# Performance work log

Measured on AMD Instinct MI355X. Metric: run time of the kernel, lower is better.

The kernel has to match this reference:

```python
import jax, jax.numpy as jnp
import numpy as np

B, T, E = 2, 2048, 2048
H, NOPE, ROPE, VD, KVR, DR = 16, 64, 32, 64, 256, 2
QKD = NOPE + ROPE  # 96
LOWR = KVR // 4    # hypernet low_rank=4 -> 64


def _rope_angles(position, dim):
    # freqs_cis angles: pos * 10000^(-2i/dim), matching torch rotary with theta=10000
    inv = jnp.exp(jnp.arange(0, dim, 2, dtype=jnp.float32) * (-jnp.log(jnp.float32(10000.0)) / dim))
    return position.astype(jnp.float32)[..., None] * inv  # (1, T, dim//2)


def _apply_rotary(x, ang):
    # x: (B,T,H,D); pairs are consecutive elements (view_as_complex semantics)
    x2 = x.reshape(x.shape[:-1] + (-1, 2))
    c = jnp.cos(ang)[:, :, None, :]
    s = jnp.sin(ang)[:, :, None, :]
    xr, xi = x2[..., 0], x2[..., 1]
    return jnp.stack([xr * c - xi * s, xr * s + xi * c], axis=-1).reshape(x.shape)


def _layernorm(x, g, b, eps=1e-5):
    m = jnp.mean(x, axis=-1, keepdims=True)
    v = jnp.var(x, axis=-1, keepdims=True)
    return (x - m) * jax.lax.rsqrt(v + eps) * g + b


def _sinusoid_pe(t, d):
    pos = jnp.arange(t, dtype=jnp.float32)[:, None]
    div = jnp.exp(jnp.arange(0, d, 2, dtype=jnp.float32) * (-jnp.log(jnp.float32(10000.0)) / d))
    pe = jnp.zeros((t, d), dtype=jnp.float32)
    pe = pe.at[:, 0::2].set(jnp.sin(pos * div)).at[:, 1::2].set(jnp.cos(pos * div))
    return pe


def setup_inputs() -> dict:
    key = jax.random.key(0)
    ks = jax.random.split(key, 16)
    sd = 0.02
    return {
        "query": jax.random.normal(ks[0], (B, T, E), jnp.float32),
        "key": jax.random.normal(ks[1], (B, T, E), jnp.float32),
        "value": jax.random.normal(ks[2], (B, T, E), jnp.float32),
        "position": jnp.arange(T, dtype=jnp.int32)[None, :],
        # weights stored transposed for right-multiply (x @ W)
        "wq": jax.random.normal(ks[3], (E, H * QKD), jnp.float32) * sd,
        "wkv_a": jax.random.normal(ks[4], (E, KVR + ROPE), jnp.float32) * sd,
        "kv_gamma": jnp.ones((KVR,), jnp.float32),
        "kv_beta": jnp.zeros((KVR,), jnp.float32),
        # torch layout (H*(NOPE+VD), KVR) kept for faithful view(H,-1,KVR) absorb
        "wkv_b": jax.random.normal(ks[5], (H * (NOPE + VD), KVR), jnp.float32) * sd,
        "wo": jax.random.normal(ks[6], (H * VD, E), jnp.float32) * sd,
        "fc_c_w": jax.random.normal(ks[7], (KVR, LOWR), jnp.float32) * sd,
        "fc_c_b": jnp.zeros((LOWR,), jnp.float32),
        "fc_p_w": jax.random.normal(ks[8], (KVR, LOWR), jnp.float32) * sd,
        "fc_p_b": jnp.zeros((LOWR,), jnp.float32),
    }


def reference(query, key, value, position, wq, wkv_a, kv_gamma, kv_beta, wkv_b, wo,
              fc_c_w, fc_c_b, fc_p_w, fc_p_b):
    bsz, seqlen, _ = query.shape
    # queries: low-rank-free path (q_lora_rank=0)
    q = (query @ wq).reshape(bsz, seqlen, H, QKD)
    q_nope, q_pe = q[..., :NOPE], q[..., NOPE:]
    ang = _rope_angles(position, ROPE)  # (1, T, ROPE//2)
    q_pe = _apply_rotary(q_pe, ang[:, -seqlen:])
    # key/value latent projection
    kv_all = key @ wkv_a  # (B, T, KVR+ROPE)
    kv, k_pe = kv_all[..., :KVR], kv_all[..., KVR:]
    k_pe = _apply_rotary(k_pe[:, :, None, :], ang)[:, :, 0, :]  # (B, T, ROPE)
    kv_norm = _layernorm(kv, kv_gamma, kv_beta)  # (B, T, KVR)
    # hypernetwork temporal downsampling weights (train path, T_input=kv_norm)
    t = -(-seqlen // DR)
    C = jnp.repeat(_sinusoid_pe(t, KVR), DR, axis=0)[:seqlen]  # (T, KVR)
    C2 = C @ fc_c_w + fc_c_b           # (T, LOWR)
    P2 = kv_norm @ fc_p_w + fc_p_b     # (B, T, LOWR)
    W = jax.nn.sigmoid(jnp.einsum('tc,bsc->bts', C2, P2))  # (B, T, T)
    idx = jnp.arange(seqlen)
    chunk = idx // DR
    # chunk mask: cumulative within-chunk causal accumulation
    zero_mask = ((chunk[:, None] == chunk[None, :]) & (idx[None, :] <= idx[:, None])).astype(query.dtype)
    kv_t = jnp.einsum('bts,bsc->btc', W * zero_mask, kv_norm)  # (B, T, KVR)
    # stride-aware causal mask: attend completed chunk-end slots + own in-progress slot
    allowed = (idx[None, :] == idx[:, None]) | ((idx[None, :] < idx[:, None]) & (((idx[None, :] + 1) % DR) == 0))
    attn_mask = jnp.where(allowed, jnp.float32(0.0), jnp.float32(-1e30))
    # absorbed MLA attention
    wb = wkv_b.reshape(H, NOPE + VD, KVR)
    q_abs = jnp.einsum('bshd,hdc->bshc', q_nope, wb[:, :NOPE])  # (B, S, H, KVR)
    scores = (jnp.einsum('bshc,btc->bsht', q_abs, kv_t)
              + jnp.einsum('bshr,btr->bsht', q_pe, k_pe)) * (QKD ** -0.5)
    scores = scores + attn_mask[None, :, None, :]
    attn = jax.nn.softmax(scores, axis=-1)
    x = jnp.einsum('bsht,btc->bshc', attn, kv_t)
    x = jnp.einsum('bshc,hdc->bshd', x, wb[:, NOPE:])  # (B, S, H, VD)
    return x.reshape(bsz, seqlen, H * VD) @ wo
```

## Files before the change

kernel.cpp:

```cpp
#include <hip/hip_runtime.h>
#include <stddef.h>

typedef unsigned short u16;
typedef unsigned short u16x8 __attribute__((ext_vector_type(8)));
typedef short s16x8 __attribute__((ext_vector_type(8)));
typedef float f32x4 __attribute__((ext_vector_type(4)));

#define B_ 2
#define T_ 2048
#define E_ 2048
#define H_ 16

__device__ inline float us2f(u16 u){
  unsigned int i = ((unsigned int)u) << 16;
  return __builtin_bit_cast(float, i);
}
__device__ inline u16 f2us(float f){
  unsigned int x = __builtin_bit_cast(unsigned int, f);
  unsigned int r = (x + 0x7fffu + ((x >> 16) & 1u)) >> 16;
  return (u16)r;
}
__device__ inline f32x4 mfma32(s16x8 a, s16x8 b, f32x4 c){
  return __builtin_amdgcn_mfma_f32_16x16x32_bf16(a, b, c, 0, 0, 0);
}
__device__ inline s16x8 ld8(const u16* p){
  return __builtin_bit_cast(s16x8, *(const u16x8*)p);
}
__device__ inline void gload_lds16(const u16* g, u16* l){
  __builtin_amdgcn_global_load_lds(
      (const __attribute__((address_space(1))) unsigned int*)(g),
      (__attribute__((address_space(3))) unsigned int*)(l), 16, 0, 0);
}

__global__ __launch_bounds__(256) void prep_weights(
    const float* __restrict__ wq, const float* __restrict__ wkva,
    const float* __restrict__ wo, const float* __restrict__ wkvb,
    u16* __restrict__ wqT, u16* __restrict__ wkvaT, u16* __restrict__ woT,
    u16* __restrict__ wkvbB)
{
  __shared__ float tile[32][33];
  const int bid = blockIdx.x;
  const int tid = threadIdx.x;
  if (bid < 5696) {
    const float* in; u16* out; int R, C, bx, by;
    if (bid < 3072)      { in = wq;   out = wqT;   R = 2048; C = 1536; bx = bid % 48;          by = bid / 48; }
    else if (bid < 3648) { in = wkva; out = wkvaT; R = 2048; C = 288;  bx = (bid-3072) % 9;    by = (bid-3072) / 9; }
    else                 { in = wo;   out = woT;   R = 1024; C = 2048; bx = (bid-3648) % 64;   by = (bid-3648) / 64; }
    int tx = tid & 31, ty = tid >> 5;
    int c0 = bx * 32, r0 = by * 32;
    for (int i = ty; i < 32; i += 8){
      int r = r0 + i, c = c0 + tx;
      tile[i][tx] = (r < R && c < C) ? in[(size_t)r * C + c] : 0.f;
    }
    __syncthreads();
    for (int i = ty; i < 32; i += 8){
      int c = c0 + i, r = r0 + tx;
      if (c < C && r < R) out[(size_t)c * R + r] = f2us(tile[tx][i]);
    }
  } else {
    int i = (bid - 5696) * 1024 + tid * 4;
    f32x4 v = *(const f32x4*)(wkvb + i);
    wkvbB[i]   = f2us(v[0]); wkvbB[i+1] = f2us(v[1]);
    wkvbB[i+2] = f2us(v[2]); wkvbB[i+3] = f2us(v[3]);
  }
}

__global__ __launch_bounds__(256) void cvt2_f32_bf16(const float* __restrict__ a,
    const float* __restrict__ b, u16* __restrict__ oa, u16* __restrict__ ob, int n_each)
{
  int idx = (blockIdx.x * 256 + threadIdx.x) * 4;
  const float* in; u16* out; int i;
  if (idx < n_each){ in = a; out = oa; i = idx; }
  else             { in = b; out = ob; i = idx - n_each; }
  if (i + 3 < n_each){
    f32x4 v = *(const f32x4*)(in + i);
    out[i]   = f2us(v[0]); out[i+1] = f2us(v[1]);
    out[i+2] = f2us(v[2]); out[i+3] = f2us(v[3]);
  }
}

template<int A_F32, int OUT_F32>
__global__ __launch_bounds__(256) void gemm_bt(const void* __restrict__ Ap,
    const u16* __restrict__ Bt, void* __restrict__ Cp, int M, int N, int K)
{
  __shared__ __align__(16) u16 As[64][40];
  __shared__ __align__(16) u16 Bs[64][40];
  const int tid  = threadIdx.x;
  const int lane = tid & 63;
  const int wid  = tid >> 6;
  const int quad = lane >> 4;
  const int col  = lane & 15;
  const int bm = blockIdx.y * 64;
  const int bn = blockIdx.x * 64;
  const int lr = tid >> 2;
  const int lc = (tid & 3) * 8;
  const int waveM = wid >> 1, waveN = wid & 1;

  f32x4 acc[2][2];
  for (int i = 0; i < 2; ++i)
    for (int j = 0; j < 2; ++j)
      acc[i][j] = (f32x4){0.f, 0.f, 0.f, 0.f};

  const u16x8 zero8 = {0,0,0,0,0,0,0,0};
  const bool bok = (bn + lr) < N;
  const u16*   arow16 = (const u16*)Ap   + (size_t)(bm + lr) * K + lc;
  const float* arow32 = (const float*)Ap + (size_t)(bm + lr) * K + lc;
  const u16* brow = Bt + (size_t)(bn + lr) * K + lc;

  for (int kk = 0; kk < K; kk += 32) {
    u16x8 av;
    if (A_F32) {
      f32x4 a0 = *(const f32x4*)(arow32 + kk);
      f32x4 a1 = *(const f32x4*)(arow32 + kk + 4);
      av[0]=f2us(a0[0]); av[1]=f2us(a0[1]); av[2]=f2us(a0[2]); av[3]=f2us(a0[3]);
      av[4]=f2us(a1[0]); av[5]=f2us(a1[1]); av[6]=f2us(a1[2]); av[7]=f2us(a1[3]);
    } else {
      av = *(const u16x8*)(arow16 + kk);
    }
    u16x8 bv = bok ? *(const u16x8*)(brow + kk) : zero8;
    __syncthreads();
    *(u16x8*)&As[lr][lc] = av;
    *(u16x8*)&Bs[lr][lc] = bv;
    __syncthreads();
    s16x8 af0 = ld8(&As[waveM*32 + col][quad*8]);
    s16x8 af1 = ld8(&As[waveM*32 + 16 + col][quad*8]);
    s16x8 bf0 = ld8(&Bs[waveN*32 + col][quad*8]);
    s16x8 bf1 = ld8(&Bs[waveN*32 + 16 + col][quad*8]);
    acc[0][0] = mfma32(af0, bf0, acc[0][0]);
    acc[0][1] = mfma32(af0, bf1, acc[0][1]);
    acc[1][0] = mfma32(af1, bf0, acc[1][0]);
    acc[1][1] = mfma32(af1, bf1, acc[1][1]);
  }
  for (int am = 0; am < 2; ++am)
    for (int bnn = 0; bnn < 2; ++bnn)
      for (int i = 0; i < 4; ++i) {
        int r = bm + waveM*32 + am*16 + quad*4 + i;
        int c = bn + waveN*32 + bnn*16 + col;
        if (c < N){
          if (OUT_F32) ((float*)Cp)[(size_t)r * N + c] = acc[am][bnn][i];
          else         ((u16*)Cp)[(size_t)r * N + c]   = f2us(acc[am][bnn][i]);
        }
      }
}

template<int OUT_F32>
__global__ __launch_bounds__(256) void gemm128(const u16* __restrict__ A,
    const u16* __restrict__ Bt, void* __restrict__ Cp, int M, int N, int K)
{
  __shared__ __align__(16) u16 As[128 * 32];
  __shared__ __align__(16) u16 Bs[128 * 32];
  const int tid  = threadIdx.x;
  const int lane = tid & 63;
  const int wid  = tid >> 6;
  const int quad = lane >> 4;
  const int col  = lane & 15;
  const int bm = blockIdx.y * 128;
  const int bn = blockIdx.x * 128;
  const int waveM = wid >> 1, waveN = wid & 1;

  const int srow = wid * 16 + (lane >> 2);
  const int scol = (lane & 3) * 8;
  const u16* ga = A  + (size_t)(bm + srow) * K + scol;
  const u16* gb = Bt + (size_t)(bn + srow) * K + scol;
  const size_t rowskip = (size_t)64 * K;
  u16* lAs0 = &As[wid * 512];
  u16* lAs1 = &As[wid * 512 + 2048];
  u16* lBs0 = &Bs[wid * 512];
  u16* lBs1 = &Bs[wid * 512 + 2048];

  f32x4 acc[4][4] = {};

  for (int kk = 0; kk < K; kk += 32) {
    __syncthreads();
    gload_lds16(ga + kk,           lAs0);
    gload_lds16(ga + rowskip + kk, lAs1);
    gload_lds16(gb + kk,           lBs0);
    gload_lds16(gb + rowskip + kk, lBs1);
    __syncthreads();
    s16x8 af[4], bf[4];
#pragma unroll
    for (int i = 0; i < 4; ++i) af[i] = ld8(&As[(waveM*64 + i*16 + col) * 32 + quad*8]);
#pragma unroll
    for (int i = 0; i < 4; ++i) bf[i] = ld8(&Bs[(waveN*64 + i*16 + col) * 32 + quad*8]);
#pragma unroll
    for (int i = 0; i < 4; ++i)
#pragma unroll
      for (int j = 0; j < 4; ++j)
        acc[i][j] = mfma32(af[i], bf[j], acc[i][j]);
  }
#pragma unroll
  for (int i = 0; i < 4; ++i)
#pragma unroll
    for (int j = 0; j < 4; ++j)
#pragma unroll
      for (int r = 0; r < 4; ++r) {
        int row = bm + waveM*64 + i*16 + quad*4 + r;
        int c   = bn + waveN*64 + j*16 + col;
        if (OUT_F32) ((float*)Cp)[(size_t)row * N + c] = acc[i][j][r];
        else         ((u16*)Cp)[(size_t)row * N + c]   = f2us(acc[i][j][r]);
      }
}

__global__ __launch_bounds__(256) void gemm128_sk(const u16* __restrict__ A,
    const u16* __restrict__ Bt, u16* __restrict__ Cp0, u16* __restrict__ Cp1,
    int M, int N, int K, int Klen)
{
  __shared__ __align__(16) u16 As[128 * 32];
  __shared__ __align__(16) u16 Bs[128 * 32];
  const int tid  = threadIdx.x;
  const int lane = tid & 63;
  const int wid  = tid >> 6;
  const int quad = lane >> 4;
  const int col  = lane & 15;
  const int bm = blockIdx.y * 128;
  const int bn = blockIdx.x * 128;
  const int kh = blockIdx.z;
  const int waveM = wid >> 1, waveN = wid & 1;

  const int srow = wid * 16 + (lane >> 2);
  const int scol = (lane & 3) * 8;
  const u16* ga = A  + (size_t)(bm + srow) * K + kh * Klen + scol;
  const u16* gb = Bt + (size_t)(bn + srow) * K + kh * Klen + scol;
  const size_t rowskip = (size_t)64 * K;
  u16* lAs0 = &As[wid * 512];
  u16* lAs1 = &As[wid * 512 + 2048];
  u16* lBs0 = &Bs[wid * 512];
  u16* lBs1 = &Bs[wid * 512 + 2048];
  u16* Cp = kh ? Cp1 : Cp0;

  f32x4 acc[4][4] = {};

  for (int kk = 0; kk < Klen; kk += 32) {
    __syncthreads();
    gload_lds16(ga + kk,           lAs0);
    gload_lds16(ga + rowskip + kk, lAs1);
    gload_lds16(gb + kk,           lBs0);
    gload_lds16(gb + rowskip + kk, lBs1);
    __syncthreads();
    s16x8 af[4], bf[4];
#pragma unroll
    for (int i = 0; i < 4; ++i) af[i] = ld8(&As[(waveM*64 + i*16 + col) * 32 + quad*8]);
#pragma unroll
    for (int i = 0; i < 4; ++i) bf[i] = ld8(&Bs[(waveN*64 + i*16 + col) * 32 + quad*8]);
#pragma unroll
    for (int i = 0; i < 4; ++i)
#pragma unroll
      for (int j = 0; j < 4; ++j)
        acc[i][j] = mfma32(af[i], bf[j], acc[i][j]);
  }
#pragma unroll
  for (int i = 0; i < 4; ++i)
#pragma unroll
    for (int j = 0; j < 4; ++j)
#pragma unroll
      for (int r = 0; r < 4; ++r) {
        int row = bm + waveM*64 + i*16 + quad*4 + r;
        int c   = bn + waveN*64 + j*16 + col;
        Cp[(size_t)row * N + c] = f2us(acc[i][j][r]);
      }
}

__global__ __launch_bounds__(256) void qsplit(const u16* __restrict__ qp0,
    const u16* __restrict__ qp1, const int* __restrict__ pos, u16* __restrict__ qh)
{
  int idx = blockIdx.x * 256 + threadIdx.x;
  if (idx >= B_*T_*H_*12) return;
  int c    = idx % 12;
  int rest = idx / 12;
  int h    = rest & 15;
  int row  = rest >> 4;
  int t    = row & (T_ - 1);
  int b    = row >> 11;
  size_t off = (size_t)row * 1536 + h * 96 + c * 8;
  u16x8 v0 = *(const u16x8*)(qp0 + off);
  u16x8 v1 = *(const u16x8*)(qp1 + off);
  u16x8 v;
  if (c < 8) {
#pragma unroll
    for (int k = 0; k < 8; ++k) v[k] = f2us(us2f(v0[k]) + us2f(v1[k]));
  } else {
    int i0 = (c - 8) * 4;
    float pp = (float)pos[t];
#pragma unroll
    for (int k = 0; k < 4; ++k){
      int i = i0 + k;
      float ang = pp * __expf((float)(2*i) * -0.28782313657f);
      float cs = __cosf(ang), sn = __sinf(ang);
      float xr = us2f(v0[2*k])   + us2f(v1[2*k]);
      float xi = us2f(v0[2*k+1]) + us2f(v1[2*k+1]);
      v[2*k]   = f2us(xr * cs - xi * sn);
      v[2*k+1] = f2us(xr * sn + xi * cs);
    }
  }
  u16* dst = qh + ((size_t)(b * 16 + h) * T_ + t) * 96;
  *(u16x8*)(dst + c * 8) = v;
}

__global__ __launch_bounds__(256) void ln_p2_rope(
    const u16* __restrict__ kvall, const float* __restrict__ gamma,
    const float* __restrict__ beta, const float* __restrict__ fcpw,
    const float* __restrict__ fcpb, const int* __restrict__ pos,
    u16* __restrict__ kvn, float* __restrict__ P2, u16* __restrict__ kpe)
{
  const int row = blockIdx.x;
  if (row >= B_ * T_) return;
  const int tid = threadIdx.x;
  const int lane = tid & 63, wid = tid >> 6;
  __shared__ float kvs[256];
  __shared__ float part[256];
  __shared__ float redS[4], redS2[4];
  const u16* src = kvall + (size_t)row * 288;
  float v = us2f(src[tid]);
  float s1 = v, s2 = v * v;
  for (int off = 1; off < 64; off <<= 1){
    s1 += __shfl_xor(s1, off);
    s2 += __shfl_xor(s2, off);
  }
  if (lane == 0){ redS[wid] = s1; redS2[wid] = s2; }
  __syncthreads();
  float S  = redS[0] + redS[1] + redS[2] + redS[3];
  float Q  = redS2[0] + redS2[1] + redS2[2] + redS2[3];
  float mean = S * (1.f / 256.f);
  float var  = Q * (1.f / 256.f) - mean * mean;
  float rstd = rsqrtf(var + 1e-5f);
  float xn = (v - mean) * rstd * gamma[tid] + beta[tid];
  kvs[tid] = xn;
  kvn[(size_t)row * 256 + tid] = f2us(xn);
  __syncthreads();
  {
    int oc = tid & 63, pp = tid >> 6;
    float acc = 0.f;
#pragma unroll 8
    for (int c = pp * 64; c < pp * 64 + 64; ++c)
      acc += kvs[c] * fcpw[c * 64 + oc];
    part[tid] = acc;
  }
  __syncthreads();
  if (tid < 64) {
    P2[(size_t)row * 64 + tid] = fcpb[tid] + part[tid] + part[64 + tid]
                               + part[128 + tid] + part[192 + tid];
  } else if (tid < 80) {
    int i = tid - 64;
    int t = row & (T_ - 1);
    float ang = (float)pos[t] * __expf((float)(2*i) * -0.28782313657f);
    float c = __cosf(ang), s = __sinf(ang);
    float xr = us2f(src[256 + 2*i]);
    float xi = us2f(src[257 + 2*i]);
    kpe[(size_t)row * 32 + 2*i]     = f2us(xr * c - xi * s);
    kpe[(size_t)row * 32 + 2*i + 1] = f2us(xr * s + xi * c);
  }
}

__global__ __launch_bounds__(256) void c2_kernel(const float* __restrict__ fccw,
    const float* __restrict__ fccb, float* __restrict__ C2)
{
  const int t = blockIdx.x, tid = threadIdx.x;
  __shared__ float pe[256];
  __shared__ float part[256];
  float p = (float)(t >> 1);
  if (tid < 128){
    float div = __expf((float)(2*tid) * -0.03597789207f);
    float a = p * div;
    pe[2*tid]   = __sinf(a);
    pe[2*tid+1] = __cosf(a);
  }
  __syncthreads();
  {
    int oc = tid & 63, pp = tid >> 6;
    float acc = 0.f;
#pragma unroll 8
    for (int c = pp * 64; c < pp * 64 + 64; ++c)
      acc += pe[c] * fccw[c * 64 + oc];
    part[tid] = acc;
  }
  __syncthreads();
  if (tid < 64)
    C2[t * 64 + tid] = fccb[tid] + part[tid] + part[64 + tid]
                     + part[128 + tid] + part[192 + tid];
}

__global__ __launch_bounds__(64) void kvt_kernel(const float* __restrict__ C2,
    const float* __restrict__ P2, const u16* __restrict__ kvn, u16* __restrict__ kvt)
{
  const int row = blockIdx.x;
  if (row >= B_ * T_) return;
  const int lane = threadIdx.x;
  const int t = row & (T_ - 1);
  float c2v = C2[t * 64 + lane];
  float da = c2v * P2[(size_t)row * 64 + lane];
  for (int off = 1; off < 64; off <<= 1) da += __shfl_xor(da, off);
  float wtt = 1.f / (1.f + __expf(-da));
  const bool odd = (t & 1);
  float wts = 0.f;
  if (odd){
    float db = c2v * P2[(size_t)(row - 1) * 64 + lane];
    for (int off = 1; off < 64; off <<= 1) db += __shfl_xor(db, off);
    wts = 1.f / (1.f + __expf(-db));
  }
  for (int c = lane; c < 256; c += 64){
    float val = wtt * us2f(kvn[(size_t)row * 256 + c]);
    if (odd) val += wts * us2f(kvn[(size_t)(row - 1) * 256 + c]);
    kvt[(size_t)row * 256 + c] = f2us(val);
  }
}

__global__ __launch_bounds__(256) void vtkc_kernel(const u16* __restrict__ kvb,
    const u16* __restrict__ kpe, u16* __restrict__ Vt, u16* __restrict__ Kc)
{
  __shared__ __align__(16) u16 tile[64][72];
  const int tid = threadIdx.x;
  if (blockIdx.x < 512) {
    const int bid = blockIdx.x;
    const int jt = bid & 15;
    const int h  = (bid >> 4) & 15;
    const int b  = bid >> 8;
    const int jl = tid >> 2;
    const int dseg = (tid & 3) * 16;
    const int j0 = jt * 64;
    {
      int s_ = 2 * (j0 + jl) + 1;
      const u16* src = kvb + ((size_t)(b * T_ + s_)) * 2048 + h * 128 + 64 + dseg;
      *(u16x8*)&tile[jl][dseg]     = *(const u16x8*)(src);
      *(u16x8*)&tile[jl][dseg + 8] = *(const u16x8*)(src + 8);
    }
    __syncthreads();
    const int dl = tid >> 2;
    const int jseg = (tid & 3) * 16;
    u16* dst = Vt + ((size_t)(b * 16 + h) * 64 + dl) * 1024 + j0 + jseg;
    u16x8 o;
    for (int r = 0; r < 8; ++r) o[r] = tile[jseg + r][dl];
    *(u16x8*)dst = o;
    for (int r = 0; r < 8; ++r) o[r] = tile[jseg + 8 + r][dl];
    *(u16x8*)(dst + 8) = o;
  } else {
    int idx = (blockIdx.x - 512) * 256 + tid;
    int c  = idx % 12;
    int j  = (idx / 12) & 1023;
    int bh = idx / (12 * 1024);
    if (bh >= B_ * H_) return;
    int b = bh >> 4, h = bh & 15;
    int t = 2 * j + 1;
    u16x8 v;
    if (c < 8) v = *(const u16x8*)(kvb + ((size_t)(b * T_ + t)) * 2048 + h * 128 + c * 8);
    else       v = *(const u16x8*)(kpe + ((size_t)(b * T_ + t)) * 32 + (c - 8) * 8);
    *(u16x8*)(Kc + ((size_t)bh * 1024 + j) * 96 + c * 8) = v;
  }
}

__global__ __launch_bounds__(256) void attn_kernel(
    const u16* __restrict__ qh, const u16* __restrict__ kvb,
    const u16* __restrict__ kpe, const u16* __restrict__ Kc,
    const u16* __restrict__ Vt, u16* __restrict__ xout)
{
  __shared__ __align__(16) u16 Ks[128 * 96];
  __shared__ __align__(16) u16 Vs[64][136];
  __shared__ __align__(16) u16 pbufA[4][16 * 136];
  const int tid  = threadIdx.x;
  const int wid  = tid >> 6;
  const int lane = tid & 63;
  const int quad = lane >> 4;
  const int col  = lane & 15;
  const int pair = blockIdx.x & 15;
  const int h    = (blockIdx.x >> 4) & 15;
  const int b    = blockIdx.x >> 8;
  const int bh   = b * H_ + h;
  u16* pbuf = pbufA[wid];
  const float scale = 0.10206207262f;
  const u16* KcH = Kc + (size_t)bh * 1024 * 96;
  const u16* VtH = Vt + (size_t)bh * 64 * 1024;

  for (int ph = 0; ph < 2; ++ph) {
    const int qt = ph ? (31 - pair) : pair;
    const int t0 = qt * 64 + wid * 16;

    s16x8 aq0, aq1, aq2;
    {
      const u16* qrow = qh + ((size_t)bh * T_ + t0 + col) * 96;
      aq0 = ld8(qrow + quad * 8);
      aq1 = ld8(qrow + 32 + quad * 8);
      aq2 = ld8(qrow + 64 + quad * 8);
    }
    float sself;
    {
      const int t = t0 + col;
      const u16* qrow = qh + ((size_t)bh * T_ + t) * 96;
      const u16* ka = kvb + ((size_t)(b * T_ + t)) * 2048 + h * 128;
      const u16* kp = kpe + ((size_t)(b * T_ + t)) * 32;
      float a = 0.f;
      for (int d = 0; d < 64; ++d) a += us2f(qrow[d]) * us2f(ka[d]);
      for (int d = 0; d < 32; ++d) a += us2f(qrow[64 + d]) * us2f(kp[d]);
      sself = a * scale;
    }
    float es[4], lacc[4];
    f32x4 O[4];
#pragma unroll
    for (int i = 0; i < 4; ++i){
      es[i] = __expf(__shfl(sself, quad * 4 + i));
      lacc[i] = 0.f;
    }
#pragma unroll
    for (int nt = 0; nt < 4; ++nt)
#pragma unroll
      for (int i = 0; i < 4; ++i){
        int t = t0 + quad * 4 + i;
        O[nt][i] = es[i] * us2f(kvb[((size_t)(b * T_ + t)) * 2048 + h * 128 + 64 + nt * 16 + col]);
      }

    const int nb = (qt * 32 + 31 + 127) >> 7;
    for (int blk = 0; blk < nb; ++blk) {
      const int jb = blk * 128;
      __syncthreads();
      {
        const u16* gk = KcH + (size_t)jb * 96 + (size_t)(wid * 6) * 512 + lane * 8;
        u16* lk = &Ks[(wid * 6) * 512];
#pragma unroll
        for (int k = 0; k < 6; ++k)
          gload_lds16(gk + k * 512, lk + k * 512);
        int d = tid >> 2, c4 = tid & 3;
        const u16* gv = VtH + (size_t)d * 1024 + jb + c4 * 32;
        u16* lv = &Vs[d][c4 * 32];
#pragma unroll
        for (int k = 0; k < 4; ++k)
          *(u16x8*)(lv + k * 8) = *(const u16x8*)(gv + k * 8);
      }
      __syncthreads();
#pragma unroll
      for (int cc = 0; cc < 4; ++cc){
        const u16* k0 = &Ks[(cc * 32 + col) * 96];
        const u16* k1 = &Ks[(cc * 32 + 16 + col) * 96];
        f32x4 s0 = {0,0,0,0}, s1 = {0,0,0,0};
        s0 = mfma32(aq0, ld8(k0 + quad * 8), s0);
        s0 = mfma32(aq1, ld8(k0 + 32 + quad * 8), s0);
        s0 = mfma32(aq2, ld8(k0 + 64 + quad * 8), s0);
        s1 = mfma32(aq0, ld8(k1 + quad * 8), s1);
        s1 = mfma32(aq1, ld8(k1 + 32 + quad * 8), s1);
        s1 = mfma32(aq2, ld8(k1 + 64 + quad * 8), s1);
        int key0 = jb + cc * 32 + col;
#pragma unroll
        for (int i = 0; i < 4; ++i){
          int lim = (t0 + quad * 4 + i) >> 1;
          float p0 = (key0 < lim)      ? __expf(s0[i] * scale) : 0.f;
          float p1 = (key0 + 16 < lim) ? __expf(s1[i] * scale) : 0.f;
          lacc[i] += p0 + p1;
          pbuf[(quad * 4 + i) * 136 + cc * 32 + col]      = f2us(p0);
          pbuf[(quad * 4 + i) * 136 + cc * 32 + 16 + col] = f2us(p1);
        }
      }
      asm volatile("s_waitcnt lgkmcnt(0)" ::: "memory");
#pragma unroll
      for (int cc = 0; cc < 4; ++cc){
        s16x8 pf = ld8(&pbuf[col * 136 + cc * 32 + quad * 8]);
#pragma unroll
        for (int nt = 0; nt < 4; ++nt)
          O[nt] = mfma32(pf, ld8(&Vs[nt * 16 + col][cc * 32 + quad * 8]), O[nt]);
      }
    }
#pragma unroll
    for (int i = 0; i < 4; ++i){
      float l = lacc[i];
      l += __shfl_xor(l, 1);
      l += __shfl_xor(l, 2);
      l += __shfl_xor(l, 4);
      l += __shfl_xor(l, 8);
      lacc[i] = es[i] + l;
    }
#pragma unroll
    for (int nt = 0; nt < 4; ++nt)
#pragma unroll
      for (int i = 0; i < 4; ++i){
        int t = t0 + quad * 4 + i;
        xout[((size_t)(b * T_ + t)) * 1024 + h * 64 + nt * 16 + col] = f2us(O[nt][i] / lacc[i]);
      }
    __syncthreads();
  }
}

extern "C" void kernel_launch(void* const* d_in, const int* in_sizes, int n_in,
                              void* d_out, int out_size, void* d_ws, size_t ws_size,
                              hipStream_t stream)
{
  (void)in_sizes; (void)n_in; (void)out_size; (void)ws_size;
  const float* query = (const float*)d_in[0];
  const float* key_  = (const float*)d_in[1];
  const int*   pos   = (const int*)d_in[3];
  const float* wq    = (const float*)d_in[4];
  const float* wkva  = (const float*)d_in[5];
  const float* gamma = (const float*)d_in[6];
  const float* beta  = (const float*)d_in[7];
  const float* wkvb  = (const float*)d_in[8];
  const float* wo    = (const float*)d_in[9];
  const float* fccw  = (const float*)d_in[10];
  const float* fccb  = (const float*)d_in[11];
  const float* fcpw  = (const float*)d_in[12];
  const float* fcpb  = (const float*)d_in[13];

  char* p = (char*)d_ws;
  auto alloc = [&](size_t bytes) -> void* {
    void* r = (void*)p;
    p += (bytes + 255) & ~(size_t)255;
    return r;
  };
  u16* wqT    = (u16*)alloc(1536ull * 2048 * 2);
  u16* wkvaT  = (u16*)alloc(288ull  * 2048 * 2);
  u16* woT    = (u16*)alloc(2048ull * 1024 * 2);
  u16* wkvbB  = (u16*)alloc(2048ull * 256 * 2);
  u16* queryB = (u16*)alloc(4096ull * 2048 * 2);
  u16* keyB   = (u16*)alloc(4096ull * 2048 * 2);
  u16* qp0    = (u16*)alloc(4096ull * 1536 * 2);
  u16* qp1    = (u16*)alloc(4096ull * 1536 * 2);
  u16* qh     = (u16*)alloc(65536ull * 96 * 2);
  u16* kvall  = (u16*)alloc(4096ull * 288 * 2);
  u16* kvn    = (u16*)alloc(4096ull * 256 * 2);
  u16* kpe    = (u16*)alloc(4096ull * 32 * 2);
  float* P2   = (float*)alloc(4096ull * 64 * 4);
  float* C2   = (float*)alloc(2048ull * 64 * 4);
  u16* kvt    = (u16*)alloc(4096ull * 256 * 2);
  u16* kvb    = (u16*)alloc(4096ull * 2048 * 2);
  u16* Kc     = (u16*)alloc(32ull * 1024 * 96 * 2);
  u16* Vt     = (u16*)alloc(2048ull * 1024 * 2);
  u16* x      = (u16*)alloc(4096ull * 1024 * 2);

  prep_weights<<<6208, 256, 0, stream>>>(wq, wkva, wo, wkvb, wqT, wkvaT, woT, wkvbB);
  cvt2_f32_bf16<<<16384, 256, 0, stream>>>(query, key_, queryB, keyB, 4096 * 2048);

  gemm128_sk<<<dim3(12, 32, 2), 256, 0, stream>>>(queryB, wqT, qp0, qp1, 4096, 1536, 2048, 1024);
  gemm_bt<0,0><<<dim3(5, 64), 256, 0, stream>>>(keyB, wkvaT, kvall, 4096, 288, 2048);

  qsplit<<<3072, 256, 0, stream>>>(qp0, qp1, pos, qh);
  ln_p2_rope<<<4096, 256, 0, stream>>>(kvall, gamma, beta, fcpw, fcpb, pos, kvn, P2, kpe);
  c2_kernel<<<2048, 256, 0, stream>>>(fccw, fccb, C2);
  kvt_kernel<<<4096, 64, 0, stream>>>(C2, P2, kvn, kvt);

  gemm128<0><<<dim3(16, 32), 256, 0, stream>>>(kvt, wkvbB, kvb, 4096, 2048, 256);
  vtkc_kernel<<<2048, 256, 0, stream>>>(kvb, kpe, Vt, Kc);
  attn_kernel<<<512, 256, 0, stream>>>(qh, kvb, kpe, Kc, Vt, x);

  gemm128<1><<<dim3(16, 32), 256, 0, stream>>>(x, woT, d_out, 4096, 2048, 1024);
}
```

Measured before the change: 364.1 us.

## Split attention into one block per query tile with smaller key tiles and swizzled K

The attention kernel now launches one block per 64-row query tile instead of pairing two tiles per block. Blocks are ordered heaviest first so the causal imbalance is handled by the scheduler rather than by pairing. Key blocks shrink from 128 to 64, which cuts LDS use so more blocks can be resident, at the cost of more loop iterations and barriers. The Kc layout gets an XOR swizzle to avoid LDS bank conflicts on the QK loads, and the self-score dot product is vectorised with 16-byte loads.

```diff
diff --git a/kernel.cpp b/kernel.cpp
--- a/kernel.cpp
+++ b/kernel.cpp
@@ -443,7 +443,9 @@
     u16x8 v;
     if (c < 8) v = *(const u16x8*)(kvb + ((size_t)(b * T_ + t)) * 2048 + h * 128 + c * 8);
     else       v = *(const u16x8*)(kpe + ((size_t)(b * T_ + t)) * 32 + (c - 8) * 8);
-    *(u16x8*)(Kc + ((size_t)bh * 1024 + j) * 96 + c * 8) = v;
+    int kl = j & 63;
+    int cs = (c & 12) | ((c & 3) ^ ((kl >> 1) & 3));
+    *(u16x8*)(Kc + ((size_t)bh * 1024 + j) * 96 + cs * 8) = v;
   }
 }
 
@@ -452,127 +454,135 @@
     const u16* __restrict__ kpe, const u16* __restrict__ Kc,
     const u16* __restrict__ Vt, u16* __restrict__ xout)
 {
-  __shared__ __align__(16) u16 Ks[128 * 96];
-  __shared__ __align__(16) u16 Vs[64][136];
-  __shared__ __align__(16) u16 pbufA[4][16 * 136];
+  __shared__ __align__(16) u16 Ks[64 * 96];
+  __shared__ __align__(16) u16 Vs[64][72];
+  __shared__ __align__(16) u16 pbufA[4][16 * 72];
   const int tid  = threadIdx.x;
   const int wid  = tid >> 6;
   const int lane = tid & 63;
   const int quad = lane >> 4;
   const int col  = lane & 15;
-  const int pair = blockIdx.x & 15;
-  const int h    = (blockIdx.x >> 4) & 15;
-  const int b    = blockIdx.x >> 8;
-  const int bh   = b * H_ + h;
+  const int qt   = 31 - (blockIdx.x >> 5);
+  const int bh   = blockIdx.x & 31;
+  const int b    = bh >> 4;
+  const int h    = bh & 15;
   u16* pbuf = pbufA[wid];
   const float scale = 0.10206207262f;
   const u16* KcH = Kc + (size_t)bh * 1024 * 96;
   const u16* VtH = Vt + (size_t)bh * 64 * 1024;
-
-  for (int ph = 0; ph < 2; ++ph) {
-    const int qt = ph ? (31 - pair) : pair;
-    const int t0 = qt * 64 + wid * 16;
-
-    s16x8 aq0, aq1, aq2;
+  const int t0 = qt * 64 + wid * 16;
+  const int qo = (quad * 8) ^ (((col >> 1) & 3) << 3);
+
+  s16x8 aq0, aq1, aq2;
+  {
+    const u16* qrow = qh + ((size_t)bh * T_ + t0 + col) * 96;
+    aq0 = ld8(qrow + quad * 8);
+    aq1 = ld8(qrow + 32 + quad * 8);
+    aq2 = ld8(qrow + 64 + quad * 8);
+  }
+  float sself;
+  {
+    const int t = t0 + col;
+    const u16* qrow = qh + ((size_t)bh * T_ + t) * 96;
+    const u16* ka = kvb + ((size_t)(b * T_ + t)) * 2048 + h * 128;
+    const u16* kp = kpe + ((size_t)(b * T_ + t)) * 32;
+    float a = 0.f;
+#pragma unroll
+    for (int c = 0; c < 8; ++c){
+      u16x8 qv = *(const u16x8*)(qrow + c * 8);
+      u16x8 kv = *(const u16x8*)(ka + c * 8);
+#pragma unroll
+      for (int jj = 0; jj < 8; ++jj) a += us2f(qv[jj]) * us2f(kv[jj]);
+    }
+#pragma unroll
+    for (int c = 0; c < 4; ++c){
+      u16x8 qv = *(const u16x8*)(qrow + 64 + c * 8);
+      u16x8 kv = *(const u16x8*)(kp + c * 8);
+#pragma unroll
+      for (int jj = 0; jj < 8; ++jj) a += us2f(qv[jj]) * us2f(kv[jj]);
+    }
+    sself = a * scale;
+  }
+  float es[4], lacc[4];
+  f32x4 O[4];
+#pragma unroll
+  for (int i = 0; i < 4; ++i){
+    es[i] = __expf(__shfl(sself, quad * 4 + i));
+    lacc[i] = 0.f;
+  }
+#pragma unroll
+  for (int nt = 0; nt < 4; ++nt)
+#pragma unroll
+    for (int i = 0; i < 4; ++i){
+      int t = t0 + quad * 4 + i;
+      O[nt][i] = es[i] * us2f(kvb[((size_t)(b * T_ + t)) * 2048 + h * 128 + 64 + nt * 16 + col]);
+    }
+
+  const int nb = (qt * 32 + 94) >> 6;
+  for (int blk = 0; blk < nb; ++blk) {
+    const int jb = blk * 64;
+    __syncthreads();
     {
-      const u16* qrow = qh + ((size_t)bh * T_ + t0 + col) * 96;
-      aq0 = ld8(qrow + quad * 8);
-      aq1 = ld8(qrow + 32 + quad * 8);
-      aq2 = ld8(qrow + 64 + quad * 8);
-    }
-    float sself;
-    {
-      const int t = t0 + col;
-      const u16* qrow = qh + ((size_t)bh * T_ + t) * 96;
-      const u16* ka = kvb + ((size_t)(b * T_ + t)) * 2048 + h * 128;
-      const u16* kp = kpe + ((size_t)(b * T_ + t)) * 32;
-      float a = 0.f;
-      for (int d = 0; d < 64; ++d) a += us2f(qrow[d]) * us2f(ka[d]);
-      for (int d = 0; d < 32; ++d) a += us2f(qrow[64 + d]) * us2f(kp[d]);
-      sself = a * scale;
-    }
-    float es[4], lacc[4];
-    f32x4 O[4];
+      const u16* gk = KcH + (size_t)jb * 96 + (wid * 3) * 512 + lane * 8;
+      u16* lk = &Ks[(wid * 3) * 512];
+#pragma unroll
+      for (int k = 0; k < 3; ++k)
+        gload_lds16(gk + k * 512, lk + k * 512);
+      int d = tid >> 2, c4 = tid & 3;
+      const u16* gv = VtH + (size_t)d * 1024 + jb + c4 * 16;
+      u16* lv = &Vs[d][c4 * 16];
+      *(u16x8*)(lv)     = *(const u16x8*)(gv);
+      *(u16x8*)(lv + 8) = *(const u16x8*)(gv + 8);
+    }
+    __syncthreads();
+#pragma unroll
+    for (int cc = 0; cc < 2; ++cc){
+      const u16* k0 = &Ks[(cc * 32 + col) * 96];
+      const u16* k1 = k0 + 16 * 96;
+      f32x4 s0 = {0,0,0,0}, s1 = {0,0,0,0};
+      s0 = mfma32(aq0, ld8(k0 + qo), s0);
+      s0 = mfma32(aq1, ld8(k0 + 32 + qo), s0);
+      s0 = mfma32(aq2, ld8(k0 + 64 + qo), s0);
+      s1 = mfma32(aq0, ld8(k1 + qo), s1);
+      s1 = mfma32(aq1, ld8(k1 + 32 + qo), s1);
+      s1 = mfma32(aq2, ld8(k1 + 64 + qo), s1);
+      int key0 = jb + cc * 32 + col;
+#pragma unroll
+      for (int i = 0; i < 4; ++i){
+        int lim = (t0 + quad * 4 + i) >> 1;
+        float p0 = (key0 < lim)      ? __expf(s0[i] * scale) : 0.f;
+        float p1 = (key0 + 16 < lim) ? __expf(s1[i] * scale) : 0.f;
+        lacc[i] += p0 + p1;
+        pbuf[(quad * 4 + i) * 72 + cc * 32 + col]      = f2us(p0);
+        pbuf[(quad * 4 + i) * 72 + cc * 32 + 16 + col] = f2us(p1);
+      }
+    }
+    asm volatile("s_waitcnt lgkmcnt(0)" ::: "memory");
+    __builtin_amdgcn_sched_barrier(0);
+#pragma unroll
+    for (int cc = 0; cc < 2; ++cc){
+      s16x8 pf = ld8(&pbuf[col * 72 + cc * 32 + quad * 8]);
+#pragma unroll
+      for (int nt = 0; nt < 4; ++nt)
+        O[nt] = mfma32(pf, ld8(&Vs[nt * 16 + col][cc * 32 + quad * 8]), O[nt]);
+    }
+  }
+#pragma unroll
+  for (int i = 0; i < 4; ++i){
+    float l = lacc[i];
+    l += __shfl_xor(l, 1);
+    l += __shfl_xor(l, 2);
+    l += __shfl_xor(l, 4);
+    l += __shfl_xor(l, 8);
+    lacc[i] = es[i] + l;
+  }
+#pragma unroll
+  for (int nt = 0; nt < 4; ++nt)
 #pragma unroll
     for (int i = 0; i < 4; ++i){
-      es[i] = __expf(__shfl(sself, quad * 4 + i));
-      lacc[i] = 0.f;
-    }
-#pragma unroll
-    for (int nt = 0; nt < 4; ++nt)
-#pragma unroll
-      for (int i = 0; i < 4; ++i){
-        int t = t0 + quad * 4 + i;
-        O[nt][i] = es[i] * us2f(kvb[((size_t)(b * T_ + t)) * 2048 + h * 128 + 64 + nt * 16 + col]);
-      }
-
-    const int nb = (qt * 32 + 31 + 127) >> 7;
-    for (int blk = 0; blk < nb; ++blk) {
-      const int jb = blk * 128;
-      __syncthreads();
-      {
-        const u16* gk = KcH + (size_t)jb * 96 + (size_t)(wid * 6) * 512 + lane * 8;
-        u16* lk = &Ks[(wid * 6) * 512];
-#pragma unroll
-        for (int k = 0; k < 6; ++k)
-          gload_lds16(gk + k * 512, lk + k * 512);
-        int d = tid >> 2, c4 = tid & 3;
-        const u16* gv = VtH + (size_t)d * 1024 + jb + c4 * 32;
-        u16* lv = &Vs[d][c4 * 32];
-#pragma unroll
-        for (int k = 0; k < 4; ++k)
-          *(u16x8*)(lv + k * 8) = *(const u16x8*)(gv + k * 8);
-      }
-      __syncthreads();
-#pragma unroll
-      for (int cc = 0; cc < 4; ++cc){
-        const u16* k0 = &Ks[(cc * 32 + col) * 96];
-        const u16* k1 = &Ks[(cc * 32 + 16 + col) * 96];
-        f32x4 s0 = {0,0,0,0}, s1 = {0,0,0,0};
-        s0 = mfma32(aq0, ld8(k0 + quad * 8), s0);
-        s0 = mfma32(aq1, ld8(k0 + 32 + quad * 8), s0);
-        s0 = mfma32(aq2, ld8(k0 + 64 + quad * 8), s0);
-        s1 = mfma32(aq0, ld8(k1 + quad * 8), s1);
-        s1 = mfma32(aq1, ld8(k1 + 32 + quad * 8), s1);
-        s1 = mfma32(aq2, ld8(k1 + 64 + quad * 8), s1);
-        int key0 = jb + cc * 32 + col;
-#pragma unroll
-        for (int i = 0; i < 4; ++i){
-          int lim = (t0 + quad * 4 + i) >> 1;
-          float p0 = (key0 < lim)      ? __expf(s0[i] * scale) : 0.f;
-          float p1 = (key0 + 16 < lim) ? __expf(s1[i] * scale) : 0.f;
-          lacc[i] += p0 + p1;
-          pbuf[(quad * 4 + i) * 136 + cc * 32 + col]      = f2us(p0);
-          pbuf[(quad * 4 + i) * 136 + cc * 32 + 16 + col] = f2us(p1);
-        }
-      }
-      asm volatile("s_waitcnt lgkmcnt(0)" ::: "memory");
-#pragma unroll
-      for (int cc = 0; cc < 4; ++cc){
-        s16x8 pf = ld8(&pbuf[col * 136 + cc * 32 + quad * 8]);
-#pragma unroll
-        for (int nt = 0; nt < 4; ++nt)
-          O[nt] = mfma32(pf, ld8(&Vs[nt * 16 + col][cc * 32 + quad * 8]), O[nt]);
-      }
-    }
-#pragma unroll
-    for (int i = 0; i < 4; ++i){
-      float l = lacc[i];
-      l += __shfl_xor(l, 1);
-      l += __shfl_xor(l, 2);
-      l += __shfl_xor(l, 4);
-      l += __shfl_xor(l, 8);
-      lacc[i] = es[i] + l;
-    }
-#pragma unroll
-    for (int nt = 0; nt < 4; ++nt)
-#pragma unroll
-      for (int i = 0; i < 4; ++i){
-        int t = t0 + quad * 4 + i;
-        xout[((size_t)(b * T_ + t)) * 1024 + h * 64 + nt * 16 + col] = f2us(O[nt][i] / lacc[i]);
-      }
-    __syncthreads();
-  }
+      int t = t0 + quad * 4 + i;
+      xout[((size_t)(b * T_ + t)) * 1024 + h * 64 + nt * 16 + col] = f2us(O[nt][i] / lacc[i]);
+    }
 }
 
 extern "C" void kernel_launch(void* const* d_in, const int* in_sizes, int n_in,
@@ -633,7 +643,7 @@
 
   gemm128<0><<<dim3(16, 32), 256, 0, stream>>>(kvt, wkvbB, kvb, 4096, 2048, 256);
   vtkc_kernel<<<2048, 256, 0, stream>>>(kvb, kpe, Vt, Kc);
-  attn_kernel<<<512, 256, 0, stream>>>(qh, kvb, kpe, Kc, Vt, x);
+  attn_kernel<<<1024, 256, 0, stream>>>(qh, kvb, kpe, Kc, Vt, x);
 
   gemm128<1><<<dim3(16, 32), 256, 0, stream>>>(x, woT, d_out, 4096, 2048, 1024);
 }
```

After: 352.3 us. 3.3% less time.
